# Kernel tuning notes

Measured on AMD Instinct MI355X. Metric: run time of the kernel, lower is better.

Reference implementation:

```python
import jax, jax.numpy as jnp
import numpy as np

N_PAIR = 32
N_ENTI = 36          # VidVRD object classes (+pad)
N_CLS_TOT = 133      # 132 predicate classes + background id 0
NUM_BASE = 92        # split='base' -> pids 1..92
N_CTX = 8
MAX_L = 40           # GeneralAlproCfg.max_txt_len
D = 768


def setup_inputs() -> dict:
    key = jax.random.key(0)
    ks = jax.random.split(key, 11)
    std = 0.02
    return {
        "so_cls_ids": jax.random.randint(ks[0], (N_PAIR, 2), 0, N_ENTI, dtype=jnp.int64),
        "enti_txt_embds": jax.random.normal(ks[1], (N_ENTI, 256), jnp.float32),
        "prefix_embds": jax.random.normal(ks[2], (N_CLS_TOT, 1, D), jnp.float32) * std,
        "suffix_embds": jax.random.normal(ks[3], (N_CLS_TOT, MAX_L - 1 - N_CTX, D), jnp.float32) * std,
        "token_mask": jnp.ones((N_CLS_TOT, MAX_L), jnp.int32),
        "meta_ctx_embds": jax.random.normal(ks[4], (N_CTX, D), jnp.float32) * std,
        "subj_ctx_embds": jax.random.normal(ks[5], (N_CTX, D), jnp.float32) * std,
        "obj_ctx_embds": jax.random.normal(ks[6], (N_CTX, D), jnp.float32) * std,
        "W1": jax.random.normal(ks[7], (512, 256), jnp.float32) * std,
        "b1": jnp.zeros((256,), jnp.float32),
        "W2": jax.random.normal(ks[8], (256, 2 * D), jnp.float32) * std,
    }


def reference(so_cls_ids, enti_txt_embds, prefix_embds, suffix_embds, token_mask,
              meta_ctx_embds, subj_ctx_embds, obj_ctx_embds, W1, b1, W2):
    n_pair = so_cls_ids.shape[0]
    pids = jnp.arange(1, NUM_BASE + 1)                      # split='base'
    n_cls = NUM_BASE

    # entity text-embedding gather + tiny MLP
    s_embd = enti_txt_embds[so_cls_ids[:, 0]]               # [n_pair, 256]
    o_embd = enti_txt_embds[so_cls_ids[:, 1]]
    so = jnp.concatenate([s_embd, o_embd], axis=-1)         # [n_pair, 512]
    h = jax.nn.relu(so @ W1 + b1)                           # [n_pair, 256]
    so_e = h @ W2                                           # [n_pair, 1536]
    s_q, o_q = so_e[:, :D], so_e[:, D:]

    # softmax attention over meta context (keys = values = meta_ctx_embds)
    scale = 1.0 / jnp.sqrt(jnp.asarray(D, jnp.float32))
    s_att = jax.nn.softmax(s_q @ meta_ctx_embds.T * scale, axis=-1) @ meta_ctx_embds  # [n_pair, D]
    o_att = jax.nn.softmax(o_q @ meta_ctx_embds.T * scale, axis=-1) @ meta_ctx_embds

    s_ctx = subj_ctx_embds[None, :, :] + s_att[:, None, :]  # [n_pair, n_ctx, D]
    o_ctx = obj_ctx_embds[None, :, :] + o_att[:, None, :]

    prefix = prefix_embds[pids]                             # [n_cls, 1, D]
    suffix = suffix_embds[pids]                             # [n_cls, L_suf, D]
    l_suf = suffix.shape[1]

    def build(ctx):
        return jnp.concatenate([
            jnp.broadcast_to(prefix[None], (n_pair, n_cls, 1, D)),
            jnp.broadcast_to(ctx[:, None], (n_pair, n_cls, N_CTX, D)),
            jnp.broadcast_to(suffix[None], (n_pair, n_cls, l_suf, D)),
        ], axis=2).reshape(n_pair * n_cls, MAX_L, D)

    subj_token_embds = build(s_ctx)                         # [n_pair*n_cls, MAX_L, D]
    obj_token_embds = build(o_ctx)
    mask = jnp.tile(token_mask[pids], (n_pair, 1))          # [n_pair*n_cls, MAX_L]
    return subj_token_embds, obj_token_embds, mask
```

## Files before the change

kernel.cpp:

```cpp
#include <hip/hip_runtime.h>
#include <hip/hip_bf16.h>

typedef unsigned int u32;
typedef __attribute__((ext_vector_type(4))) float f32x4;

#define NPAIR 32
#define NCLS  92
#define NCTX  8
#define MAXL  40
#define DIM   768
#define LSUF  31

#define MAT_ELEMS 90439680u
#define MASK_BASE 180879360u
#define NBLK_MAT  7360u
#define MASK_F4   29440u
#define NBLK_MASK 154u

#define WS_ATT  0u
#define WS_H    49152u
#define WS_SOE  57344u

__global__ __launch_bounds__(512) void k_h(
    const int* __restrict__ so_ids,
    const float* __restrict__ enti,
    const float* __restrict__ W1,
    const float* __restrict__ b1,
    float* __restrict__ ws)
{
    const int p = blockIdx.x;
    const int t = threadIdx.x;
    __shared__ float so_vec[512];
    __shared__ float w1part[2][256];
    __shared__ int ids[2];

    if (t == 0) {
        bool is64 = true;
        for (int i = 1; i < 64; i += 2) is64 = is64 && (so_ids[i] == 0);
        if (is64) { ids[0] = so_ids[4 * p];     ids[1] = so_ids[4 * p + 2]; }
        else      { ids[0] = so_ids[2 * p];     ids[1] = so_ids[2 * p + 1]; }
    }
    __syncthreads();
    so_vec[t] = (t < 256) ? enti[ids[0] * 256 + t] : enti[ids[1] * 256 + (t - 256)];
    __syncthreads();

    const int j = t & 255, half = t >> 8;
    const float* w = W1 + (half * 256) * 256 + j;
    const float* sv = so_vec + half * 256;
    float acc = 0.f;
    #pragma unroll 8
    for (int kk = 0; kk < 256; ++kk)
        acc = fmaf(sv[kk], w[(size_t)kk * 256], acc);
    w1part[half][j] = acc;
    __syncthreads();
    if (t < 256)
        ws[WS_H + p * 256 + t] = fmaxf(w1part[0][t] + w1part[1][t] + b1[t], 0.f);
}

__global__ __launch_bounds__(256) void k_soe(
    const float* __restrict__ W2,
    float* __restrict__ ws)
{
    const int p = blockIdx.x / 6;
    const int cc = blockIdx.x % 6;
    const int t = threadIdx.x;
    __shared__ float hl[256];
    hl[t] = ws[WS_H + p * 256 + t];
    __syncthreads();

    const int c = cc * 256 + t;
    const float* w = W2 + c;
    float acc = 0.f;
    #pragma unroll 8
    for (int k = 0; k < 256; ++k)
        acc = fmaf(hl[k], w[(size_t)k * 1536], acc);
    ws[WS_SOE + p * 1536 + c] = acc;
}

__global__ __launch_bounds__(256) void k_att(
    const float* __restrict__ meta,
    float* __restrict__ ws)
{
    const int which = blockIdx.x >> 5;
    const int p = blockIdx.x & 31;
    const int t = threadIdx.x;
    __shared__ float red[8][256];
    __shared__ float probs[8];

    const float* q = ws + WS_SOE + p * 1536 + which * DIM;
    float qr[3];
    #pragma unroll
    for (int i = 0; i < 3; ++i) qr[i] = q[t + 256 * i];

    #pragma unroll
    for (int c = 0; c < 8; ++c) {
        float pp = 0.f;
        #pragma unroll
        for (int i = 0; i < 3; ++i)
            pp = fmaf(qr[i], meta[c * DIM + t + 256 * i], pp);
        red[c][t] = pp;
    }
    __syncthreads();
    for (int s = 128; s > 0; s >>= 1) {
        if (t < s) {
            #pragma unroll
            for (int c = 0; c < 8; ++c)
                red[c][t] += red[c][t + s];
        }
        __syncthreads();
    }
    if (t == 0) {
        const float scale = 0.036084391824351615f;
        float sc[8], m = -1e30f;
        #pragma unroll
        for (int c = 0; c < 8; ++c) { sc[c] = red[c][0] * scale; m = fmaxf(m, sc[c]); }
        float sum = 0.f;
        #pragma unroll
        for (int c = 0; c < 8; ++c) { sc[c] = expf(sc[c] - m); sum += sc[c]; }
        const float inv = 1.f / sum;
        #pragma unroll
        for (int c = 0; c < 8; ++c) probs[c] = sc[c] * inv;
    }
    __syncthreads();
    #pragma unroll
    for (int i = 0; i < 3; ++i) {
        const int d = t + 256 * i;
        float a = 0.f;
        #pragma unroll
        for (int c = 0; c < 8; ++c)
            a = fmaf(probs[c], meta[c * DIM + d], a);
        ws[WS_ATT + (which * NPAIR + p) * DIM + d] = a;
    }
}

__global__ __launch_bounds__(192) void k_build(
    const float* __restrict__ prefix,
    const float* __restrict__ suffix,
    const int* __restrict__ tok_mask,
    const float* __restrict__ sctx,
    const float* __restrict__ octx,
    const float* __restrict__ att,
    float* __restrict__ out)
{
    const u32 bid = blockIdx.x;
    const u32 t = threadIdx.x;

    if (bid < NBLK_MAT) {
        const u32 which = bid / 3680u;
        const u32 rem = bid - which * 3680u;
        const u32 cls = rem / 40u;
        const u32 tok = rem - cls * 40u;
        const u32 d = t * 4u;

        f32x4 src;
        bool is_ctx = false;
        if (tok == 0u) {
            src = *(const f32x4*)(prefix + (cls + 1u) * DIM + d);
        } else if (tok < 9u) {
            const float* cp = (which ? octx : sctx) + (tok - 1u) * DIM + d;
            src = *(const f32x4*)cp;
            is_ctx = true;
        } else {
            src = *(const f32x4*)(suffix + ((cls + 1u) * LSUF + (tok - 9u)) * DIM + d);
        }

        float* base = out + (size_t)which * MAT_ELEMS + (size_t)(cls * MAXL + tok) * DIM + d;
        const float* ab = att + (size_t)which * NPAIR * DIM + d;
        if (is_ctx) {
            #pragma unroll 4
            for (u32 p = 0; p < NPAIR; ++p) {
                const f32x4 a = *(const f32x4*)(ab + (size_t)p * DIM);
                __builtin_nontemporal_store(src + a,
                    (f32x4*)(base + (size_t)p * (NCLS * MAXL * DIM)));
            }
        } else {
            #pragma unroll 4
            for (u32 p = 0; p < NPAIR; ++p) {
                __builtin_nontemporal_store(src,
                    (f32x4*)(base + (size_t)p * (NCLS * MAXL * DIM)));
            }
        }
    } else {
        const u32 idx4 = (bid - NBLK_MAT) * 192u + t;
        if (idx4 < MASK_F4) {
            const u32 m = idx4 * 4u;
            f32x4 v;
            #pragma unroll
            for (int j = 0; j < 4; ++j) {
                const u32 i = m + (u32)j;
                const u32 rw = i / 40u;
                const u32 tk = i - rw * 40u;
                const u32 cls = rw % 92u;
                v[j] = (float)tok_mask[(cls + 1u) * 40u + tk];
            }
            __builtin_nontemporal_store(v, (f32x4*)(out + MASK_BASE + m));
        }
    }
}

extern "C" void kernel_launch(void* const* d_in, const int* in_sizes, int n_in,
                              void* d_out, int out_size, void* d_ws, size_t ws_size,
                              hipStream_t stream) {
    const int* so_ids     = (const int*)d_in[0];
    const float* enti     = (const float*)d_in[1];
    const float* prefix   = (const float*)d_in[2];
    const float* suffix   = (const float*)d_in[3];
    const int* tok_mask   = (const int*)d_in[4];
    const float* meta     = (const float*)d_in[5];
    const float* sctx     = (const float*)d_in[6];
    const float* octx     = (const float*)d_in[7];
    const float* W1       = (const float*)d_in[8];
    const float* b1       = (const float*)d_in[9];
    const float* W2       = (const float*)d_in[10];
    float* ws = (float*)d_ws;

    k_h  <<<dim3(NPAIR), dim3(512), 0, stream>>>(so_ids, enti, W1, b1, ws);
    k_soe<<<dim3(192),   dim3(256), 0, stream>>>(W2, ws);
    k_att<<<dim3(64),    dim3(256), 0, stream>>>(meta, ws);
    k_build<<<dim3(NBLK_MAT + NBLK_MASK), dim3(192), 0, stream>>>(
        prefix, suffix, tok_mask, sctx, octx, ws + WS_ATT, (float*)d_out);
}
```

Measured before the change: 166.6 us.

## Remap build kernel to one block per (pair, class) row writing contiguous output

The build kernel switches from one block per (class, token) that loops over all 32 pairs with large-stride stores to one block per (which, pair, class) that writes a contiguous 40x768 slab. The pair's attention vector is staged in shared memory and added to the context tokens. Each block now produces one contiguous region instead of 32 scattered rows, which should improve store coalescing and DRAM page locality. In exchange, prefix, suffix and context source data are re-read by every pair instead of being loaded once, and each block adds a shared-memory sync.

```diff
diff --git a/kernel.cpp b/kernel.cpp
--- a/kernel.cpp
+++ b/kernel.cpp
@@ -13,9 +13,9 @@
 
 #define MAT_ELEMS 90439680u
 #define MASK_BASE 180879360u
-#define NBLK_MAT  7360u
+#define NBLK_MAT  5888u
 #define MASK_F4   29440u
-#define NBLK_MASK 154u
+#define NBLK_MASK 115u
 
 #define WS_ATT  0u
 #define WS_H    49152u
@@ -133,7 +133,7 @@
     }
 }
 
-__global__ __launch_bounds__(192) void k_build(
+__global__ __launch_bounds__(256) void k_build(
     const float* __restrict__ prefix,
     const float* __restrict__ suffix,
     const int* __restrict__ tok_mask,
@@ -146,42 +146,40 @@
     const u32 t = threadIdx.x;
 
     if (bid < NBLK_MAT) {
-        const u32 which = bid / 3680u;
-        const u32 rem = bid - which * 3680u;
-        const u32 cls = rem / 40u;
-        const u32 tok = rem - cls * 40u;
-        const u32 d = t * 4u;
-
-        f32x4 src;
-        bool is_ctx = false;
-        if (tok == 0u) {
-            src = *(const f32x4*)(prefix + (cls + 1u) * DIM + d);
-        } else if (tok < 9u) {
-            const float* cp = (which ? octx : sctx) + (tok - 1u) * DIM + d;
-            src = *(const f32x4*)cp;
-            is_ctx = true;
-        } else {
-            src = *(const f32x4*)(suffix + ((cls + 1u) * LSUF + (tok - 9u)) * DIM + d);
-        }
-
-        float* base = out + (size_t)which * MAT_ELEMS + (size_t)(cls * MAXL + tok) * DIM + d;
-        const float* ab = att + (size_t)which * NPAIR * DIM + d;
-        if (is_ctx) {
-            #pragma unroll 4
-            for (u32 p = 0; p < NPAIR; ++p) {
-                const f32x4 a = *(const f32x4*)(ab + (size_t)p * DIM);
-                __builtin_nontemporal_store(src + a,
-                    (f32x4*)(base + (size_t)p * (NCLS * MAXL * DIM)));
+        const u32 which = bid / (NPAIR * NCLS);
+        const u32 rem = bid - which * (NPAIR * NCLS);
+        const u32 pair = rem / NCLS;
+        const u32 cls = rem - pair * NCLS;
+
+        __shared__ __align__(16) float attl[DIM];
+        for (u32 i = t; i < DIM; i += 256u)
+            attl[i] = att[(which * NPAIR + pair) * DIM + i];
+        __syncthreads();
+
+        const float* ctx = which ? octx : sctx;
+        const f32x4* pre4 = (const f32x4*)(prefix + (cls + 1u) * DIM);
+        const f32x4* suf4 = (const f32x4*)(suffix + (size_t)(cls + 1u) * LSUF * DIM);
+        f32x4* base4 = (f32x4*)(out + (size_t)which * MAT_ELEMS
+                                    + ((size_t)pair * NCLS + cls) * (MAXL * DIM));
+
+        #pragma unroll 6
+        for (u32 it = 0; it < 30u; ++it) {
+            const u32 chunk = it * 256u + t;
+            const u32 tok = chunk / 192u;
+            const u32 dpos = chunk - tok * 192u;
+            f32x4 v;
+            if (tok == 0u) {
+                v = pre4[dpos];
+            } else if (tok < 9u) {
+                v = *(const f32x4*)(ctx + (tok - 1u) * DIM + dpos * 4u)
+                  + *(const f32x4*)(attl + dpos * 4u);
+            } else {
+                v = suf4[(tok - 9u) * 192u + dpos];
             }
-        } else {
-            #pragma unroll 4
-            for (u32 p = 0; p < NPAIR; ++p) {
-                __builtin_nontemporal_store(src,
-                    (f32x4*)(base + (size_t)p * (NCLS * MAXL * DIM)));
-            }
+            __builtin_nontemporal_store(v, base4 + chunk);
         }
     } else {
-        const u32 idx4 = (bid - NBLK_MAT) * 192u + t;
+        const u32 idx4 = (bid - NBLK_MAT) * 256u + t;
         if (idx4 < MASK_F4) {
             const u32 m = idx4 * 4u;
             f32x4 v;
@@ -217,6 +215,6 @@
     k_h  <<<dim3(NPAIR), dim3(512), 0, stream>>>(so_ids, enti, W1, b1, ws);
     k_soe<<<dim3(192),   dim3(256), 0, stream>>>(W2, ws);
     k_att<<<dim3(64),    dim3(256), 0, stream>>>(meta, ws);
-    k_build<<<dim3(NBLK_MAT + NBLK_MASK), dim3(192), 0, stream>>>(
+    k_build<<<dim3(NBLK_MAT + NBLK_MASK), dim3(256), 0, stream>>>(
         prefix, suffix, tok_mask, sctx, octx, ws + WS_ATT, (float*)d_out);
 }
```

New measurement: 173.0 us. 1.04x slower.
